# Kernel tuning notes

Measured on AMD Instinct MI355X. Metric: run time of the kernel, lower is better.

Reference implementation:

```python
import jax, jax.numpy as jnp
import numpy as np

N_NODES = 50000
N_EDGES = 250000
D_IN, D_HID, D_OUT = 768, 256, 2


def _sage_conv(x, src, dst, W_l, b_l, W_r, n_nodes):
    # PyG SAGEConv (aggr='mean', root_weight=True):
    #   out[i] = lin_l(mean_{j in N(i)} x[j]) + lin_r(x[i])
    msg = x[src]  # [E, d] gather of source-node features
    agg = jax.ops.segment_sum(msg, dst, num_segments=n_nodes)
    cnt = jax.ops.segment_sum(jnp.ones((src.shape[0],), x.dtype), dst,
                              num_segments=n_nodes)
    agg = agg / jnp.maximum(cnt, 1.0)[:, None]
    return agg @ W_l.T + b_l + x @ W_r.T


def setup_inputs() -> dict:
    key = jax.random.key(0)
    ks = jax.random.split(key, 7)
    x = jax.random.normal(ks[0], (N_NODES, D_IN), dtype=jnp.float32)
    edge_index = jax.random.randint(ks[1], (2, N_EDGES), 0, N_NODES,
                                    dtype=jnp.int64)
    s1 = 1.0 / np.sqrt(D_IN)
    s2 = 1.0 / np.sqrt(D_HID)
    W1_l = jax.random.uniform(ks[2], (D_HID, D_IN), jnp.float32, -s1, s1)
    W1_r = jax.random.uniform(ks[3], (D_HID, D_IN), jnp.float32, -s1, s1)
    b1 = jnp.zeros((D_HID,), jnp.float32)
    W2_l = jax.random.uniform(ks[4], (D_OUT, D_HID), jnp.float32, -s2, s2)
    W2_r = jax.random.uniform(ks[5], (D_OUT, D_HID), jnp.float32, -s2, s2)
    b2 = jnp.zeros((D_OUT,), jnp.float32)
    return {"x": x, "edge_index": edge_index,
            "W1_l": W1_l, "b1": b1, "W1_r": W1_r,
            "W2_l": W2_l, "b2": b2, "W2_r": W2_r}


def reference(x, edge_index, W1_l, b1, W1_r, W2_l, b2, W2_r):
    src, dst = edge_index[0], edge_index[1]
    n = x.shape[0]
    h = _sage_conv(x, src, dst, W1_l, b1, W1_r, n)
    h = jax.nn.relu(h)
    # dropout is identity in eval mode (deterministic reference)
    out = _sage_conv(h, src, dst, W2_l, b2, W2_r, n)
    return out
```

## Files before the change

kernel.cpp:

```cpp
#include <hip/hip_runtime.h>
#include <stdint.h>


#define D_IN  768
#define D_HID 256
#define N1    512

typedef __attribute__((ext_vector_type(8))) short short8;
typedef __attribute__((ext_vector_type(4))) float f32x4;

__device__ __forceinline__ void async_copy16(const void* g, void* l) {
  __builtin_amdgcn_global_load_lds(
      (const __attribute__((address_space(1))) unsigned int*)g,
      (__attribute__((address_space(3))) unsigned int*)l,
      16, 0, 0);
}

__device__ __forceinline__ unsigned short f2bf(float f) {
  union { float f; unsigned u; } v; v.f = f;
  unsigned r = v.u + 0x7FFFu + ((v.u >> 16) & 1u);
  return (unsigned short)(r >> 16);
}

__device__ __forceinline__ float bf2f(unsigned short b) {
  union { unsigned u; float f; } v; v.u = ((unsigned)b) << 16;
  return v.f;
}


__global__ void detect_k(const unsigned int* __restrict__ w,
                         unsigned int* __restrict__ flag, int E) {
  int i = blockIdx.x * 256 + threadIdx.x;
  unsigned v = (i < E) ? w[2 * i + 1] : 0u;
  unsigned long long any = __ballot(v != 0u);
  if ((threadIdx.x & 63) == 0 && any) atomicOr(flag, 1u);
}

__global__ void cvtidx_k(const void* __restrict__ eidx,
                         const unsigned int* __restrict__ flag,
                         int* __restrict__ src32, int* __restrict__ dst32,
                         int* __restrict__ counts, int E) {
  int i = blockIdx.x * 256 + threadIdx.x;
  if (i >= E) return;
  int s, d;
  if (*flag) {
    const int* p = (const int*)eidx;
    s = p[i]; d = p[E + i];
  } else {
    const long long* p = (const long long*)eidx;
    s = (int)p[i]; d = (int)p[E + i];
  }
  src32[i] = s;
  dst32[i] = d;
  atomicAdd(&counts[d], 1);
}

__global__ void scanA_k(const int* __restrict__ counts,
                        int* __restrict__ blockSums, int M) {
  __shared__ int ts[256];
  int b = blockIdx.x, t = threadIdx.x;
  int base = b * 1024 + t * 4;
  int s = 0;
#pragma unroll
  for (int k = 0; k < 4; k++) { int i = base + k; if (i < M) s += counts[i]; }
  ts[t] = s;
  __syncthreads();
  for (int off = 128; off > 0; off >>= 1) {
    if (t < off) ts[t] += ts[t + off];
    __syncthreads();
  }
  if (t == 0) blockSums[b] = ts[0];
}

__global__ void scanC_k(const int* __restrict__ counts,
                        const int* __restrict__ bsums,
                        int* __restrict__ offs, int* __restrict__ cursor,
                        int M, int E, int nb) {
  __shared__ int ts[256];
  __shared__ int bofs;
  int b = blockIdx.x, t = threadIdx.x;
  if (t < 64) {
    int v = (t < nb) ? bsums[t] : 0;
    int orig = v;
#pragma unroll
    for (int off = 1; off < 64; off <<= 1) {
      int u = __shfl_up(v, off);
      if (t >= off) v += u;
    }
    if (t == b) bofs = v - orig;
  }
  int base = b * 1024 + t * 4;
  int v[4]; int s = 0;
#pragma unroll
  for (int k = 0; k < 4; k++) {
    int i = base + k;
    v[k] = (i < M) ? counts[i] : 0;
    s += v[k];
  }
  ts[t] = s;
  __syncthreads();
  for (int off = 1; off < 256; off <<= 1) {
    int x = (t >= off) ? ts[t - off] : 0;
    __syncthreads();
    ts[t] += x;
    __syncthreads();
  }
  int run = bofs + ts[t] - s;
#pragma unroll
  for (int k = 0; k < 4; k++) {
    int i = base + k;
    if (i < M) { offs[i] = run; cursor[i] = run; run += v[k]; }
  }
  if (b == 0 && t == 0) offs[M] = E;
}

__global__ void fill_k(const int* __restrict__ src, const int* __restrict__ dst,
                       int* __restrict__ cursor, int* __restrict__ csr, int E) {
  int i = blockIdx.x * 256 + threadIdx.x;
  if (i >= E) return;
  int pos = atomicAdd(&cursor[dst[i]], 1);
  csr[pos] = src[i];
}


__global__ void cvtw_k(const float* __restrict__ W1l, const float* __restrict__ W1r,
                       unsigned short* __restrict__ wb) {
  int idx = blockIdx.x * 256 + threadIdx.x;
  int total = N1 * (D_IN / 8);
  if (idx >= total) return;
  int row = idx / (D_IN / 8);
  int cpos = (idx % (D_IN / 8)) * 8;
  const float* p = (row < D_HID) ? (W1l + (size_t)row * D_IN + cpos)
                                 : (W1r + (size_t)(row - D_HID) * D_IN + cpos);
  float4 f0 = *(const float4*)p;
  float4 f1 = *(const float4*)(p + 4);
  short8 o;
  o[0] = (short)f2bf(f0.x); o[1] = (short)f2bf(f0.y);
  o[2] = (short)f2bf(f0.z); o[3] = (short)f2bf(f0.w);
  o[4] = (short)f2bf(f1.x); o[5] = (short)f2bf(f1.y);
  o[6] = (short)f2bf(f1.z); o[7] = (short)f2bf(f1.w);
  *(short8*)(wb + (size_t)idx * 8) = o;
}

__global__ __launch_bounds__(256) void gemm_k(
    const float* __restrict__ x,
    const unsigned short* __restrict__ wb,
    unsigned short* __restrict__ Cb, int M) {
  __shared__ unsigned short As[128 * 32];
  __shared__ unsigned short Bs[128 * 32];
  const int tid  = threadIdx.x;
  const int lane = tid & 63;
  const int wid  = tid >> 6;
  const int wr = wid >> 1, wc = wid & 1;
  const int m0 = blockIdx.y * 128;
  const int n0 = blockIdx.x * 128;
  const int l15  = lane & 15;
  const int quad = lane >> 4;

  const int ca0 = tid, ca1 = 256 + tid;
  const int arow0 = ca0 >> 2, akg0 = ca0 & 3;
  const int arow1 = ca1 >> 2, akg1 = ca1 & 3;
  const float* agp0 = x + (size_t)min(m0 + arow0, M - 1) * D_IN + akg0 * 8;
  const float* agp1 = x + (size_t)min(m0 + arow1, M - 1) * D_IN + akg1 * 8;
  unsigned short* alp0 = &As[(arow0 >> 4) * 512 + akg0 * 128 + (arow0 & 15) * 8];
  unsigned short* alp1 = &As[(arow1 >> 4) * 512 + akg1 * 128 + (arow1 & 15) * 8];

  f32x4 acc[4][4];
#pragma unroll
  for (int r = 0; r < 4; r++)
#pragma unroll
    for (int c = 0; c < 4; c++) acc[r][c] = (f32x4)0.0f;

  for (int k0 = 0; k0 < D_IN; k0 += 32) {
    __syncthreads();
    float4 a00 = *(const float4*)(agp0 + k0);
    float4 a01 = *(const float4*)(agp0 + k0 + 4);
    float4 a10 = *(const float4*)(agp1 + k0);
    float4 a11 = *(const float4*)(agp1 + k0 + 4);
#pragma unroll
    for (int l = 0; l < 2; ++l) {
      int cb = l * 256 + tid;
      int row = (cb >> 6) * 16 + (cb & 15);
      int cg  = (cb >> 4) & 3;
      async_copy16(wb + (size_t)(n0 + row) * D_IN + k0 + cg * 8, &Bs[cb * 8]);
    }
    short8 o0, o1;
    o0[0] = (short)f2bf(a00.x); o0[1] = (short)f2bf(a00.y);
    o0[2] = (short)f2bf(a00.z); o0[3] = (short)f2bf(a00.w);
    o0[4] = (short)f2bf(a01.x); o0[5] = (short)f2bf(a01.y);
    o0[6] = (short)f2bf(a01.z); o0[7] = (short)f2bf(a01.w);
    o1[0] = (short)f2bf(a10.x); o1[1] = (short)f2bf(a10.y);
    o1[2] = (short)f2bf(a10.z); o1[3] = (short)f2bf(a10.w);
    o1[4] = (short)f2bf(a11.x); o1[5] = (short)f2bf(a11.y);
    o1[6] = (short)f2bf(a11.z); o1[7] = (short)f2bf(a11.w);
    *(short8*)alp0 = o0;
    *(short8*)alp1 = o1;
    __syncthreads();

    short8 a[4], b[4];
#pragma unroll
    for (int r = 0; r < 4; r++)
      a[r] = *(const short8*)&As[(wr * 4 + r) * 512 + quad * 128 + l15 * 8];
#pragma unroll
    for (int c = 0; c < 4; c++)
      b[c] = *(const short8*)&Bs[(wc * 4 + c) * 512 + quad * 128 + l15 * 8];
#pragma unroll
    for (int r = 0; r < 4; r++)
#pragma unroll
      for (int c = 0; c < 4; c++)
        acc[r][c] = __builtin_amdgcn_mfma_f32_16x16x32_bf16(a[r], b[c], acc[r][c], 0, 0, 0);
  }

  const int crow0 = m0 + wr * 64;
  const int ccol0 = n0 + wc * 64;
#pragma unroll
  for (int r = 0; r < 4; r++)
#pragma unroll
    for (int c = 0; c < 4; c++) {
      int col = ccol0 + c * 16 + l15;
#pragma unroll
      for (int reg = 0; reg < 4; reg++) {
        int row = crow0 + r * 16 + quad * 4 + reg;
        Cb[(size_t)row * N1 + col] = f2bf(acc[r][c][reg]);
      }
    }
}

__global__ void agg_l2_k(const unsigned short* __restrict__ Cb,
                         const int* __restrict__ offs, const int* __restrict__ csr,
                         const float* __restrict__ b1,
                         const float* __restrict__ W2l, const float* __restrict__ W2r,
                         float4* __restrict__ rs, int M) {
  int tid = threadIdx.x;
  int lane = tid & 63;
  int wid = tid >> 6;
  int wave = blockIdx.x * 4 + wid;
  int nw = gridDim.x * 4;
  int c = lane * 4;
  float4 bv  = *(const float4*)(b1 + c);
  float4 wl0 = *(const float4*)(W2l + c);
  float4 wl1 = *(const float4*)(W2l + D_HID + c);
  float4 wr0 = *(const float4*)(W2r + c);
  float4 wr1 = *(const float4*)(W2r + D_HID + c);
  for (int i = wave; i < M; i += nw) {
    int s = offs[i], e = offs[i + 1];
    float ax = 0.f, ay = 0.f, az = 0.f, aw = 0.f;
    for (int t = s; t < e; t++) {
      int j = csr[t];
      ushort4 v = *(const ushort4*)(Cb + (size_t)j * N1 + c);
      ax += bf2f(v.x); ay += bf2f(v.y); az += bf2f(v.z); aw += bf2f(v.w);
    }
    float inv = 1.0f / fmaxf((float)(e - s), 1.0f);
    ushort4 q = *(const ushort4*)(Cb + (size_t)i * N1 + D_HID + c);
    float h0 = fmaxf(ax * inv + bv.x + bf2f(q.x), 0.0f);
    float h1 = fmaxf(ay * inv + bv.y + bf2f(q.y), 0.0f);
    float h2 = fmaxf(az * inv + bv.z + bf2f(q.z), 0.0f);
    float h3 = fmaxf(aw * inv + bv.w + bf2f(q.w), 0.0f);
    float r0 = h0 * wl0.x + h1 * wl0.y + h2 * wl0.z + h3 * wl0.w;
    float r1 = h0 * wl1.x + h1 * wl1.y + h2 * wl1.z + h3 * wl1.w;
    float s0 = h0 * wr0.x + h1 * wr0.y + h2 * wr0.z + h3 * wr0.w;
    float s1 = h0 * wr1.x + h1 * wr1.y + h2 * wr1.z + h3 * wr1.w;
#pragma unroll
    for (int off = 32; off > 0; off >>= 1) {
      r0 += __shfl_xor(r0, off);
      r1 += __shfl_xor(r1, off);
      s0 += __shfl_xor(s0, off);
      s1 += __shfl_xor(s1, off);
    }
    if (lane == 0) rs[i] = make_float4(r0, r1, s0, s1);
  }
}

__global__ void final_k(const float4* __restrict__ rs, const int* __restrict__ offs,
                        const int* __restrict__ csr, const float* __restrict__ b2,
                        float* __restrict__ out, int M) {
  int i = blockIdx.x * 256 + threadIdx.x;
  if (i >= M) return;
  int s = offs[i], e = offs[i + 1];
  float a0 = 0.0f, a1 = 0.0f;
  for (int t = s; t < e; t++) {
    float4 v = rs[csr[t]];
    a0 += v.x; a1 += v.y;
  }
  float inv = 1.0f / fmaxf((float)(e - s), 1.0f);
  float4 me = rs[i];
  out[2 * i + 0] = a0 * inv + b2[0] + me.z;
  out[2 * i + 1] = a1 * inv + b2[1] + me.w;
}


extern "C" void kernel_launch(void* const* d_in, const int* in_sizes, int n_in,
                              void* d_out, int out_size, void* d_ws, size_t ws_size,
                              hipStream_t stream) {
  const float* x   = (const float*)d_in[0];
  const void*  eix = d_in[1];
  const float* W1l = (const float*)d_in[2];
  const float* b1  = (const float*)d_in[3];
  const float* W1r = (const float*)d_in[4];
  const float* W2l = (const float*)d_in[5];
  const float* b2  = (const float*)d_in[6];
  const float* W2r = (const float*)d_in[7];
  float* out = (float*)d_out;

  const int M  = in_sizes[0] / D_IN;
  const int E  = in_sizes[1] / 2;
  const int Mp = ((M + 127) / 128) * 128;
  const int nb = (M + 1023) / 1024;

  char* ws = (char*)d_ws;
  size_t off = 0;
  auto alloc = [&](size_t b) { size_t o = off; off += (b + 255) & ~(size_t)255; return o; };
  size_t oFlag   = alloc(4);
  size_t oCounts = alloc((size_t)M * 4);
  size_t zeroBytes = oCounts + (size_t)M * 4;
  size_t oOffs   = alloc((size_t)(M + 1) * 4);
  size_t oCursor = alloc((size_t)M * 4);
  size_t oCsr    = alloc((size_t)E * 4);
  size_t oSrc    = alloc((size_t)E * 4);
  size_t oDst    = alloc((size_t)E * 4);
  size_t oBSums  = alloc(64 * 4);
  size_t oWb     = alloc((size_t)N1 * D_IN * 2);
  size_t oC      = alloc((size_t)Mp * N1 * 2);
  size_t oRs     = alloc((size_t)M * 16);
  (void)ws_size; (void)n_in; (void)out_size;

  unsigned int* flag = (unsigned int*)(ws + oFlag);
  int* counts = (int*)(ws + oCounts);
  int* offs   = (int*)(ws + oOffs);
  int* cursor = (int*)(ws + oCursor);
  int* csr    = (int*)(ws + oCsr);
  int* src32  = (int*)(ws + oSrc);
  int* dst32  = (int*)(ws + oDst);
  int* bsums  = (int*)(ws + oBSums);
  unsigned short* wb = (unsigned short*)(ws + oWb);
  unsigned short* Cb = (unsigned short*)(ws + oC);
  float4* rs = (float4*)(ws + oRs);

  hipMemsetAsync(ws, 0, zeroBytes, stream);

  int gE = (E + 255) / 256;
  detect_k<<<gE, 256, 0, stream>>>((const unsigned int*)eix, flag, E);
  cvtidx_k<<<gE, 256, 0, stream>>>(eix, flag, src32, dst32, counts, E);
  scanA_k<<<nb, 256, 0, stream>>>(counts, bsums, M);
  scanC_k<<<nb, 256, 0, stream>>>(counts, bsums, offs, cursor, M, E, nb);
  fill_k<<<gE, 256, 0, stream>>>(src32, dst32, cursor, csr, E);

  int gW = (N1 * (D_IN / 8) + 255) / 256;
  cvtw_k<<<gW, 256, 0, stream>>>(W1l, W1r, wb);

  dim3 gg(N1 / 128, Mp / 128);
  gemm_k<<<gg, 256, 0, stream>>>(x, wb, Cb, M);

  agg_l2_k<<<2048, 256, 0, stream>>>(Cb, offs, csr, b1, W2l, W2r, rs, M);
  final_k<<<(M + 255) / 256, 256, 0, stream>>>(rs, offs, csr, b2, out, M);
}
```

Before: 435.2 us.

## Double-buffer GEMM LDS tiles with prefetch, swizzle A, fuse index-width detection

The GEMM kernel now keeps two LDS buffers. It prefetches the next K-slice of x into registers and the next slice of weights via async global-to-LDS copies while the MFMAs run on the current slice, which removes one barrier per iteration and overlaps load latency with compute. The A tile's row index is XOR-swizzled by k-group to reduce LDS bank conflicts. The separate detect_k kernel is folded into cvtidx_k as a per-block ballot with a shared flag, which drops one launch and the flag memset. The cost is that index-width detection is now per block rather than global, so a block of int32 data whose high words are all zero would be misread.

After: 388.6 us. 1.12x faster.

```diff
diff --git a/kernel.cpp b/kernel.cpp
--- a/kernel.cpp
+++ b/kernel.cpp
@@ -5,6 +5,7 @@
 #define D_IN  768
 #define D_HID 256
 #define N1    512
+#define KITERS (D_IN / 32)
 
 typedef __attribute__((ext_vector_type(8))) short short8;
 typedef __attribute__((ext_vector_type(4))) float f32x4;
@@ -28,22 +29,21 @@
 }
 
 
-__global__ void detect_k(const unsigned int* __restrict__ w,
-                         unsigned int* __restrict__ flag, int E) {
-  int i = blockIdx.x * 256 + threadIdx.x;
-  unsigned v = (i < E) ? w[2 * i + 1] : 0u;
-  unsigned long long any = __ballot(v != 0u);
-  if ((threadIdx.x & 63) == 0 && any) atomicOr(flag, 1u);
-}
-
 __global__ void cvtidx_k(const void* __restrict__ eidx,
-                         const unsigned int* __restrict__ flag,
                          int* __restrict__ src32, int* __restrict__ dst32,
                          int* __restrict__ counts, int E) {
-  int i = blockIdx.x * 256 + threadIdx.x;
+  __shared__ int flag32;
+  int tid = threadIdx.x;
+  int i = blockIdx.x * 256 + tid;
+  unsigned v = (i < E) ? ((const unsigned int*)eidx)[2 * (size_t)i + 1] : 0u;
+  unsigned long long any = __ballot(v != 0u);
+  if (tid == 0) flag32 = 0;
+  __syncthreads();
+  if ((tid & 63) == 0 && any) flag32 = 1;
+  __syncthreads();
   if (i >= E) return;
   int s, d;
-  if (*flag) {
+  if (flag32) {
     const int* p = (const int*)eidx;
     s = p[i]; d = p[E + i];
   } else {
@@ -146,8 +146,8 @@
     const float* __restrict__ x,
     const unsigned short* __restrict__ wb,
     unsigned short* __restrict__ Cb, int M) {
-  __shared__ unsigned short As[128 * 32];
-  __shared__ unsigned short Bs[128 * 32];
+  __shared__ unsigned short As[2][128 * 32];
+  __shared__ unsigned short Bs[2][128 * 32];
   const int tid  = threadIdx.x;
   const int lane = tid & 63;
   const int wid  = tid >> 6;
@@ -157,13 +157,21 @@
   const int l15  = lane & 15;
   const int quad = lane >> 4;
 
-  const int ca0 = tid, ca1 = 256 + tid;
-  const int arow0 = ca0 >> 2, akg0 = ca0 & 3;
-  const int arow1 = ca1 >> 2, akg1 = ca1 & 3;
-  const float* agp0 = x + (size_t)min(m0 + arow0, M - 1) * D_IN + akg0 * 8;
-  const float* agp1 = x + (size_t)min(m0 + arow1, M - 1) * D_IN + akg1 * 8;
-  unsigned short* alp0 = &As[(arow0 >> 4) * 512 + akg0 * 128 + (arow0 & 15) * 8];
-  unsigned short* alp1 = &As[(arow1 >> 4) * 512 + akg1 * 128 + (arow1 & 15) * 8];
+  const int arow0 = tid >> 2, akg = tid & 3;
+  const int arow1 = arow0 + 64;
+  const int aswz = akg | ((akg & 1) << 2);
+  const float* agp0 = x + (size_t)min(m0 + arow0, M - 1) * D_IN + akg * 8;
+  const float* agp1 = x + (size_t)min(m0 + arow1, M - 1) * D_IN + akg * 8;
+  const int aoff0 = (arow0 >> 4) * 512 + akg * 128 + ((arow0 & 15) ^ aswz) * 8;
+  const int aoff1 = (arow1 >> 4) * 512 + akg * 128 + ((arow1 & 15) ^ aswz) * 8;
+  const int pquad = quad | ((quad & 1) << 2);
+
+  const int brow = (tid >> 6) * 16 + (tid & 15);
+  const int bcg  = (tid >> 4) & 3;
+  const unsigned short* bgp0 = wb + (size_t)(n0 + brow) * D_IN + bcg * 8;
+  const unsigned short* bgp1 = wb + (size_t)(n0 + brow + 64) * D_IN + bcg * 8;
+  const int boff0 = tid * 8;
+  const int boff1 = (tid + 256) * 8;
 
   f32x4 acc[4][4];
 #pragma unroll
@@ -171,19 +179,15 @@
 #pragma unroll
     for (int c = 0; c < 4; c++) acc[r][c] = (f32x4)0.0f;
 
-  for (int k0 = 0; k0 < D_IN; k0 += 32) {
-    __syncthreads();
-    float4 a00 = *(const float4*)(agp0 + k0);
-    float4 a01 = *(const float4*)(agp0 + k0 + 4);
-    float4 a10 = *(const float4*)(agp1 + k0);
-    float4 a11 = *(const float4*)(agp1 + k0 + 4);
-#pragma unroll
-    for (int l = 0; l < 2; ++l) {
-      int cb = l * 256 + tid;
-      int row = (cb >> 6) * 16 + (cb & 15);
-      int cg  = (cb >> 4) & 3;
-      async_copy16(wb + (size_t)(n0 + row) * D_IN + k0 + cg * 8, &Bs[cb * 8]);
-    }
+  float4 a00 = *(const float4*)(agp0);
+  float4 a01 = *(const float4*)(agp0 + 4);
+  float4 a10 = *(const float4*)(agp1);
+  float4 a11 = *(const float4*)(agp1 + 4);
+  async_copy16(bgp0, &Bs[0][boff0]);
+  async_copy16(bgp1, &Bs[0][boff1]);
+
+  for (int it = 0; it < KITERS; ++it) {
+    const int p = it & 1;
     short8 o0, o1;
     o0[0] = (short)f2bf(a00.x); o0[1] = (short)f2bf(a00.y);
     o0[2] = (short)f2bf(a00.z); o0[3] = (short)f2bf(a00.w);
@@ -193,17 +197,28 @@
     o1[2] = (short)f2bf(a10.z); o1[3] = (short)f2bf(a10.w);
     o1[4] = (short)f2bf(a11.x); o1[5] = (short)f2bf(a11.y);
     o1[6] = (short)f2bf(a11.z); o1[7] = (short)f2bf(a11.w);
-    *(short8*)alp0 = o0;
-    *(short8*)alp1 = o1;
+    *(short8*)&As[p][aoff0] = o0;
+    *(short8*)&As[p][aoff1] = o1;
+
     __syncthreads();
 
+    if (it + 1 < KITERS) {
+      const int k1 = (it + 1) * 32;
+      a00 = *(const float4*)(agp0 + k1);
+      a01 = *(const float4*)(agp0 + k1 + 4);
+      a10 = *(const float4*)(agp1 + k1);
+      a11 = *(const float4*)(agp1 + k1 + 4);
+      async_copy16(bgp0 + k1, &Bs[p ^ 1][boff0]);
+      async_copy16(bgp1 + k1, &Bs[p ^ 1][boff1]);
+    }
+
     short8 a[4], b[4];
 #pragma unroll
     for (int r = 0; r < 4; r++)
-      a[r] = *(const short8*)&As[(wr * 4 + r) * 512 + quad * 128 + l15 * 8];
+      a[r] = *(const short8*)&As[p][(wr * 4 + r) * 512 + quad * 128 + ((l15 ^ pquad)) * 8];
 #pragma unroll
     for (int c = 0; c < 4; c++)
-      b[c] = *(const short8*)&Bs[(wc * 4 + c) * 512 + quad * 128 + l15 * 8];
+      b[c] = *(const short8*)&Bs[p][(wc * 4 + c) * 512 + quad * 128 + l15 * 8];
 #pragma unroll
     for (int r = 0; r < 4; r++)
 #pragma unroll
@@ -310,9 +325,8 @@
   char* ws = (char*)d_ws;
   size_t off = 0;
   auto alloc = [&](size_t b) { size_t o = off; off += (b + 255) & ~(size_t)255; return o; };
-  size_t oFlag   = alloc(4);
   size_t oCounts = alloc((size_t)M * 4);
-  size_t zeroBytes = oCounts + (size_t)M * 4;
+  size_t zeroBytes = (size_t)M * 4;
   size_t oOffs   = alloc((size_t)(M + 1) * 4);
   size_t oCursor = alloc((size_t)M * 4);
   size_t oCsr    = alloc((size_t)E * 4);
@@ -324,7 +338,6 @@
   size_t oRs     = alloc((size_t)M * 16);
   (void)ws_size; (void)n_in; (void)out_size;
 
-  unsigned int* flag = (unsigned int*)(ws + oFlag);
   int* counts = (int*)(ws + oCounts);
   int* offs   = (int*)(ws + oOffs);
   int* cursor = (int*)(ws + oCursor);
@@ -336,11 +349,10 @@
   unsigned short* Cb = (unsigned short*)(ws + oC);
   float4* rs = (float4*)(ws + oRs);
 
-  hipMemsetAsync(ws, 0, zeroBytes, stream);
+  hipMemsetAsync(counts, 0, zeroBytes, stream);
 
   int gE = (E + 255) / 256;
-  detect_k<<<gE, 256, 0, stream>>>((const unsigned int*)eix, flag, E);
-  cvtidx_k<<<gE, 256, 0, stream>>>(eix, flag, src32, dst32, counts, E);
+  cvtidx_k<<<gE, 256, 0, stream>>>(eix, src32, dst32, counts, E);
   scanA_k<<<nb, 256, 0, stream>>>(counts, bsums, M);
   scanC_k<<<nb, 256, 0, stream>>>(counts, bsums, offs, cursor, M, E, nb);
   fill_k<<<gE, 256, 0, stream>>>(src32, dst32, cursor, csr, E);
```
